# Optimization experiments

Hardware: AMD Instinct MI355X
Metric: run time of the kernel (lower is better)

## Reference

```python
import jax, jax.numpy as jnp
import numpy as np

B, N, C = 8, 1024, 768
H = 12
D = C // H  # head_dim = 64
SCALE = D ** -0.5
EPS = 1e-5


def _layer_norm(x):
    # per-head LayerNorm over last dim, gamma=1, beta=0, biased variance
    mean = x.mean(-1, keepdims=True)
    var = ((x - mean) ** 2).mean(-1, keepdims=True)
    return (x - mean) / jnp.sqrt(var + EPS)


def setup_inputs() -> dict:
    key = jax.random.key(0)
    k1, k2, k3 = jax.random.split(key, 3)
    x = jax.random.normal(k1, (B, N, C), dtype=jnp.float32)
    qkv_weight = jax.random.normal(k2, (3 * C, C), dtype=jnp.float32) * (C ** -0.5)
    proj_weight = jax.random.normal(k3, (C, C), dtype=jnp.float32) * (C ** -0.5)
    return {"x": x, "qkv_weight": qkv_weight, "proj_weight": proj_weight}


def reference(x, qkv_weight, proj_weight):
    Bx, Nx, Cx = x.shape
    qkv = x @ qkv_weight.T                          # [B,N,3C]
    qkv = qkv.reshape(Bx, Nx, 3, H, D).transpose(2, 0, 3, 1, 4)  # [3,B,H,N,D]
    q, k, v = qkv[0], qkv[1], qkv[2]
    q = _layer_norm(q) * SCALE
    k = _layer_norm(k)
    attn = jnp.einsum('bhnd,bhmd->bhnm', q, k)      # [B,H,N,N]
    attn = jax.nn.softmax(attn, axis=-1)
    out = jnp.einsum('bhnm,bhmd->bhnd', attn, v)    # [B,H,N,D]
    out = out.transpose(0, 2, 1, 3).reshape(Bx, Nx, Cx)
    return out @ proj_weight.T
```

## Files before the change

### kernel.cpp

```cpp
#include <hip/hip_runtime.h>
#include <stdint.h>
#include <stddef.h>

#define HB 8
#define HN 1024
#define HC 768
#define HH 12
#define HD 64
#define ROWS (HB*HN)
#define BH (HB*HH)

using s16x4  = __attribute__((ext_vector_type(4))) short;
using bf16x8 = __attribute__((ext_vector_type(8))) short;
using f32x4  = __attribute__((ext_vector_type(4))) float;

__device__ __forceinline__ short f2bf(float f) {
  union { float f; uint32_t u; } c; c.f = f;
  uint32_t u = c.u;
  uint32_t r = (u + 0x7fffu + ((u >> 16) & 1u)) >> 16;
  return (short)r;
}
__device__ __forceinline__ float bf2f(short s) {
  union { uint32_t u; float f; } c; c.u = ((uint32_t)(uint16_t)s) << 16;
  return c.f;
}
__device__ __forceinline__ uint32_t pack_bf16_rne(float a, float b) {
  union { float f; uint32_t u; } ca, cb; ca.f = a; cb.f = b;
  uint32_t ra = ca.u + 0x7fffu + ((ca.u >> 16) & 1u);
  uint32_t rb = cb.u + 0x7fffu + ((cb.u >> 16) & 1u);
  return __builtin_amdgcn_perm(rb, ra, 0x07060302);
}
__device__ __forceinline__ float fast_exp2(float x) {
#if __has_builtin(__builtin_amdgcn_exp2f)
  return __builtin_amdgcn_exp2f(x);
#else
  return exp2f(x);
#endif
}
__device__ __forceinline__ f32x4 mfma16(bf16x8 a, bf16x8 b, f32x4 c) {
  return __builtin_amdgcn_mfma_f32_16x16x32_bf16(a, b, c, 0, 0, 0);
}
__device__ __forceinline__ void gll16(const void* g, void* l) {
  __builtin_amdgcn_global_load_lds((const __attribute__((address_space(1))) void*)g,
                                   (__attribute__((address_space(3))) void*)l,
                                   16, 0, 0);
}

__global__ void cvt3_kernel(const float* __restrict__ x,  short* __restrict__ xb,  int n0,
                            const float* __restrict__ wq, short* __restrict__ wqb, int n1,
                            const float* __restrict__ wp, short* __restrict__ wpb, int n2) {
  int i = blockIdx.x * 256 + threadIdx.x;
  const float* in; short* out;
  if (i < n0)            { in = x;  out = xb;  }
  else if (i < n0 + n1)  { i -= n0; in = wq; out = wqb; }
  else if (i < n0 + n1 + n2) { i -= n0 + n1; in = wp; out = wpb; }
  else return;
  float4 v = ((const float4*)in)[i];
  s16x4 o;
  o.x = f2bf(v.x); o.y = f2bf(v.y); o.z = f2bf(v.z); o.w = f2bf(v.w);
  ((s16x4*)out)[i] = o;
}

template<int VM, bool STG, int SLOT>
__device__ __forceinline__ void qkv_ktile(
    int kt, short* sA, short* sB,
    const short* Ag, const short* Bg,
    int wr, int wc, int quad, int lc,
    int aoff0, int aoff1, int boff0,
    int cA0, int cA1, int cB0,
    f32x4 (&acc)[4][4])
{
  if constexpr (VM == 3) asm volatile("s_waitcnt vmcnt(3)" ::: "memory");
  else                   asm volatile("s_waitcnt vmcnt(0)" ::: "memory");
  __builtin_amdgcn_s_barrier();
  if constexpr (STG) {
    constexpr int DST = (SLOT + 2) % 3;
    const int kcol = (kt + 2) * 32;
    short* dA = sA + DST*8192;
    short* dB = sB + DST*4096;
    gll16(Ag + (size_t)(aoff0 + kcol), (void*)(dA + cA0*8));
    gll16(Ag + (size_t)(aoff1 + kcol), (void*)(dA + cA1*8));
    gll16(Bg + (size_t)(boff0 + kcol), (void*)(dB + cB0*8));
  }
  const short* sa = sA + SLOT*8192;
  const short* sb = sB + SLOT*4096;
  bf16x8 af[4], bfr[4];
#pragma unroll
  for (int mt = 0; mt < 4; ++mt) {
    const int rA = wr*64 + mt*16 + lc;
    af[mt] = *(const bf16x8*)(sa + rA*32 + (quad ^ ((rA >> 1) & 3))*8);
  }
#pragma unroll
  for (int nt = 0; nt < 4; ++nt) {
    const int rB = wc*64 + nt*16 + lc;
    bfr[nt] = *(const bf16x8*)(sb + rB*32 + (quad ^ ((rB >> 1) & 3))*8);
  }
  __builtin_amdgcn_s_setprio(1);
#pragma unroll
  for (int mt = 0; mt < 4; ++mt)
#pragma unroll
    for (int nt = 0; nt < 4; ++nt)
      acc[mt][nt] = mfma16(af[mt], bfr[nt], acc[mt][nt]);
  __builtin_amdgcn_s_setprio(0);
}

__global__ __launch_bounds__(512, 4) void gemm_qkv(const short* __restrict__ A,
                                                   const short* __restrict__ Bw,
                                                   short* __restrict__ Qb,
                                                   short* __restrict__ Kb,
                                                   short* __restrict__ Vtb) {
  __shared__ short SMEM[3*256*32 + 3*128*32];
  short* As = SMEM;
  short* Bs = SMEM + 3*256*32;
  const int wg = blockIdx.x;
  const int swz = (wg & 7)*72 + (wg >> 3);
  const int by = swz / 18, bx = swz % 18;
  const int m0 = by*256, n0 = bx*128;
  const int tid = threadIdx.x;
  const int lane = tid & 63, w = tid >> 6, quad = lane >> 4, lc = lane & 15;
  const int wr = w >> 1, wc = w & 1;
  const int cA0 = tid,        rA0 = cA0 >> 2, sbA0 = ((cA0 & 3) ^ ((rA0 >> 1) & 3))*8;
  const int cA1 = 512 + tid,  rA1 = cA1 >> 2, sbA1 = ((cA1 & 3) ^ ((rA1 >> 1) & 3))*8;
  const int cB0 = tid,        rB0 = cB0 >> 2, sbB0 = ((cB0 & 3) ^ ((rB0 >> 1) & 3))*8;
  const int aoff0 = rA0*HC + sbA0;
  const int aoff1 = rA1*HC + sbA1;
  const int boff0 = rB0*HC + sbB0;
  const short* Ag = A  + (size_t)m0*HC;
  const short* Bg = Bw + (size_t)n0*HC;
  f32x4 acc[4][4] = {};

#pragma unroll
  for (int pk = 0; pk < 2; ++pk) {
    gll16(Ag + (size_t)(aoff0 + pk*32), (void*)(As + pk*8192 + cA0*8));
    gll16(Ag + (size_t)(aoff1 + pk*32), (void*)(As + pk*8192 + cA1*8));
    gll16(Bg + (size_t)(boff0 + pk*32), (void*)(Bs + pk*4096 + cB0*8));
  }

#pragma unroll 1
  for (int kt = 0; kt < 21; kt += 3) {
    qkv_ktile<3,true,0>(kt,   As, Bs, Ag, Bg, wr, wc, quad, lc,
                        aoff0, aoff1, boff0, cA0, cA1, cB0, acc);
    qkv_ktile<3,true,1>(kt+1, As, Bs, Ag, Bg, wr, wc, quad, lc,
                        aoff0, aoff1, boff0, cA0, cA1, cB0, acc);
    qkv_ktile<3,true,2>(kt+2, As, Bs, Ag, Bg, wr, wc, quad, lc,
                        aoff0, aoff1, boff0, cA0, cA1, cB0, acc);
  }
  qkv_ktile<3,true ,0>(21, As, Bs, Ag, Bg, wr, wc, quad, lc,
                       aoff0, aoff1, boff0, cA0, cA1, cB0, acc);
  qkv_ktile<3,false,1>(22, As, Bs, Ag, Bg, wr, wc, quad, lc,
                       aoff0, aoff1, boff0, cA0, cA1, cB0, acc);
  qkv_ktile<0,false,2>(23, As, Bs, Ag, Bg, wr, wc, quad, lc,
                       aoff0, aoff1, boff0, cA0, cA1, cB0, acc);

  const int cg = n0 + wc*64;
  const int t = cg / HC;
  const int h = (cg % HC) / HD;
  if (t < 2) {
    short* outp = (t == 0) ? Qb : Kb;
    const float sc = (t == 0) ? 0.125f : 1.0f;
#pragma unroll
    for (int i = 0; i < 4; ++i)
#pragma unroll
      for (int r = 0; r < 4; ++r) {
        float s1 = (acc[i][0][r] + acc[i][1][r]) + (acc[i][2][r] + acc[i][3][r]);
        float s2 = acc[i][0][r]*acc[i][0][r];
        s2 = __builtin_fmaf(acc[i][1][r], acc[i][1][r], s2);
        s2 = __builtin_fmaf(acc[i][2][r], acc[i][2][r], s2);
        s2 = __builtin_fmaf(acc[i][3][r], acc[i][3][r], s2);
#pragma unroll
        for (int off = 1; off < 16; off <<= 1) {
          s1 += __shfl_xor(s1, off);
          s2 += __shfl_xor(s2, off);
        }
        const float mean = s1 * (1.0f/64.0f);
        const float var  = s2 * (1.0f/64.0f) - mean*mean;
        const float inv  = rsqrtf(var + 1e-5f) * sc;
        const int row = m0 + wr*64 + i*16 + quad*4 + r;
        const int b = row >> 10, n_in = row & 1023;
        short* rowp = outp + ((size_t)(b*HH + h)*HN + n_in)*HD;
#pragma unroll
        for (int nt = 0; nt < 4; ++nt)
          rowp[nt*16 + lc] = f2bf((acc[i][nt][r] - mean) * inv);
      }
  } else {
    short* vs = SMEM;
    __syncthreads();
    const int hd = wc;
#pragma unroll
    for (int i = 0; i < 4; ++i)
#pragma unroll
      for (int nt = 0; nt < 4; ++nt)
#pragma unroll
        for (int r = 0; r < 4; ++r) {
          const int dd = nt*16 + lc;
          const int k  = i*16 + quad*4 + r;
          const int c  = ((k & 15) << 2) | (k >> 4);
          vs[(hd*64 + dd)*268 + wr*64 + c] = f2bf(acc[i][nt][r]);
        }
    __syncthreads();
    const int b = m0 >> 10, m0g = m0 & 1023;
#pragma unroll
    for (int it = 0; it < 8; ++it) {
      const int idx = it*512 + tid;
      const int h2 = idx >> 11;
      const int rem = idx & 2047;
      const int dd = rem >> 5, c8 = rem & 31;
      const int habs = ((n0 + h2*64) - 1536) >> 6;
      const short* src = vs + (h2*64 + dd)*268 + c8*8;
      s16x4 lo = *(const s16x4*)(src);
      s16x4 hi = *(const s16x4*)(src + 4);
      bf16x8 vvv;
      vvv[0]=lo[0]; vvv[1]=lo[1]; vvv[2]=lo[2]; vvv[3]=lo[3];
      vvv[4]=hi[0]; vvv[5]=hi[1]; vvv[6]=hi[2]; vvv[7]=hi[3];
      *(bf16x8*)(Vtb + ((size_t)((b*HH + habs)*HD + dd))*HN + m0g + c8*8) = vvv;
    }
  }
}

template<int VM, bool STG, int SLOT>
__device__ __forceinline__ void bt_ktile(
    int kt, short* sA, short* sB,
    const short* Ag, const short* Bg,
    int wr, int wc, int quad, int lc,
    int aoff0, int aoff1, int boff0, int boff1,
    int cA0, int cA1, int cB0, int cB1,
    f32x4 (&acc)[4][4])
{
  if constexpr (VM == 4) asm volatile("s_waitcnt vmcnt(4)" ::: "memory");
  else                   asm volatile("s_waitcnt vmcnt(0)" ::: "memory");
  __builtin_amdgcn_s_barrier();
  if constexpr (STG) {
    constexpr int DST = (SLOT + 2) % 3;
    const int kcol = (kt + 2) * 32;
    short* dA = sA + DST*4096;
    short* dB = sB + DST*4096;
    gll16(Ag + (size_t)(aoff0 + kcol), (void*)(dA + cA0*8));
    gll16(Ag + (size_t)(aoff1 + kcol), (void*)(dA + cA1*8));
    gll16(Bg + (size_t)(boff0 + kcol), (void*)(dB + cB0*8));
    gll16(Bg + (size_t)(boff1 + kcol), (void*)(dB + cB1*8));
  }
  const short* sa = sA + SLOT*4096;
  const short* sb = sB + SLOT*4096;
  bf16x8 af[4], bfr[4];
#pragma unroll
  for (int mt = 0; mt < 4; ++mt) {
    const int rA = wr*64 + mt*16 + lc;
    af[mt] = *(const bf16x8*)(sa + rA*32 + (quad ^ ((rA >> 1) & 3))*8);
  }
#pragma unroll
  for (int nt = 0; nt < 4; ++nt) {
    const int rB = wc*64 + nt*16 + lc;
    bfr[nt] = *(const bf16x8*)(sb + rB*32 + (quad ^ ((rB >> 1) & 3))*8);
  }
  __builtin_amdgcn_s_setprio(1);
#pragma unroll
  for (int mt = 0; mt < 4; ++mt)
#pragma unroll
    for (int nt = 0; nt < 4; ++nt)
      acc[mt][nt] = mfma16(af[mt], bfr[nt], acc[mt][nt]);
  __builtin_amdgcn_s_setprio(0);
}

__global__ __launch_bounds__(256, 3) void gemm_bt_f32(const short* __restrict__ A,
                                                      const short* __restrict__ Bw,
                                                      float* __restrict__ C) {
  __shared__ short As[3*128*32];
  __shared__ short Bs[3*128*32];
  const int wg = blockIdx.x;
  const int swz = (wg & 7)*48 + (wg >> 3);
  const int by = swz / 6, bx = swz % 6;
  const int m0 = by*128, n0 = bx*128;
  const int tid = threadIdx.x;
  const int lane = tid & 63, w = tid >> 6, quad = lane >> 4, lc = lane & 15;
  const int wr = w >> 1, wc = w & 1;
  const int cA0 = tid,        rA0 = cA0 >> 2, sbA0 = ((cA0 & 3) ^ ((rA0 >> 1) & 3))*8;
  const int cA1 = 256 + tid,  rA1 = cA1 >> 2, sbA1 = ((cA1 & 3) ^ ((rA1 >> 1) & 3))*8;
  const int aoff0 = rA0*HC + sbA0;
  const int aoff1 = rA1*HC + sbA1;
  const int cB0 = cA0, cB1 = cA1;
  const int boff0 = aoff0, boff1 = aoff1;
  const short* Ag = A  + (size_t)m0*HC;
  const short* Bg = Bw + (size_t)n0*HC;
  f32x4 acc[4][4] = {};

#pragma unroll
  for (int pk = 0; pk < 2; ++pk) {
    gll16(Ag + (size_t)(aoff0 + pk*32), (void*)(As + pk*4096 + cA0*8));
    gll16(Ag + (size_t)(aoff1 + pk*32), (void*)(As + pk*4096 + cA1*8));
    gll16(Bg + (size_t)(boff0 + pk*32), (void*)(Bs + pk*4096 + cB0*8));
    gll16(Bg + (size_t)(boff1 + pk*32), (void*)(Bs + pk*4096 + cB1*8));
  }

#pragma unroll 1
  for (int kt = 0; kt < 21; kt += 3) {
    bt_ktile<4,true,0>(kt,   As, Bs, Ag, Bg, wr, wc, quad, lc,
                       aoff0, aoff1, boff0, boff1, cA0, cA1, cB0, cB1, acc);
    bt_ktile<4,true,1>(kt+1, As, Bs, Ag, Bg, wr, wc, quad, lc,
                       aoff0, aoff1, boff0, boff1, cA0, cA1, cB0, cB1, acc);
    bt_ktile<4,true,2>(kt+2, As, Bs, Ag, Bg, wr, wc, quad, lc,
                       aoff0, aoff1, boff0, boff1, cA0, cA1, cB0, cB1, acc);
  }
  bt_ktile<4,true ,0>(21, As, Bs, Ag, Bg, wr, wc, quad, lc,
                      aoff0, aoff1, boff0, boff1, cA0, cA1, cB0, cB1, acc);
  bt_ktile<4,false,1>(22, As, Bs, Ag, Bg, wr, wc, quad, lc,
                      aoff0, aoff1, boff0, boff1, cA0, cA1, cB0, cB1, acc);
  bt_ktile<0,false,2>(23, As, Bs, Ag, Bg, wr, wc, quad, lc,
                      aoff0, aoff1, boff0, boff1, cA0, cA1, cB0, cB1, acc);

#pragma unroll
  for (int mt = 0; mt < 4; ++mt)
#pragma unroll
    for (int nt = 0; nt < 4; ++nt)
#pragma unroll
      for (int r = 0; r < 4; ++r) {
        const int row = m0 + wr*64 + mt*16 + quad*4 + r;
        const int col = n0 + wc*64 + nt*16 + lc;
        C[(size_t)row*HC + col] = acc[mt][nt][r];
      }
}

__global__ __launch_bounds__(256, 3) void attn_kernel(const short* __restrict__ Qb,
                                                      const short* __restrict__ Kb,
                                                      const short* __restrict__ Vtb,
                                                      short* __restrict__ AOb) {
  const int raw = blockIdx.x;
  const int blk = (raw & 7)*96 + (raw >> 3);
  const int qt = blk & 7, bh = blk >> 3;
  const int b = bh / HH, h = bh % HH;
  const int tid = threadIdx.x, w = tid >> 6, lane = tid & 63;
  const int quad = lane >> 4, lc = lane & 15;

  __shared__ short Ks [64][72];
  __shared__ short Vts[64][72];
  __shared__ short Ps [4][32][72];

  bf16x8 aq[2][2];
#pragma unroll
  for (int mt = 0; mt < 2; ++mt) {
    const int mrow = qt*128 + w*32 + mt*16 + lc;
    aq[mt][0] = *(const bf16x8*)(Qb + ((size_t)bh*HN + mrow)*HD + quad*8);
    aq[mt][1] = *(const bf16x8*)(Qb + ((size_t)bh*HN + mrow)*HD + 32 + quad*8);
  }

  const short* kbh = Kb  + (size_t)bh*HN*HD;
  const short* vbh = Vtb + (size_t)bh*HD*HN;

  f32x4 oacc[2][4] = {};
  float l_i[2][4] = {};

  bf16x8 gk[2], gv[2];
#pragma unroll
  for (int i = 0; i < 2; ++i) {
    const int c = i*256 + tid;
    gk[i] = *(const bf16x8*)(kbh + (size_t)(c >> 3)*HD + (c & 7)*8);
    gv[i] = *(const bf16x8*)(vbh + (size_t)(c >> 3)*HN + (c & 7)*8);
  }
#pragma unroll
  for (int i = 0; i < 2; ++i) {
    const int c = i*256 + tid;
    *(bf16x8*)(&Ks [c >> 3][(c & 7)*8]) = gk[i];
    *(bf16x8*)(&Vts[c >> 3][(c & 7)*8]) = gv[i];
  }
  __syncthreads();

  const float LOG2E = 1.44269504f;
  const float MB2   = 8.0f * 1.44269504f;

  for (int ck = 0; ck < 16; ++ck) {
    if (ck < 15) {
      const int nn0 = (ck + 1)*64;
#pragma unroll
      for (int i = 0; i < 2; ++i) {
        const int c = i*256 + tid;
        gk[i] = *(const bf16x8*)(kbh + (size_t)(nn0 + (c >> 3))*HD + (c & 7)*8);
        gv[i] = *(const bf16x8*)(vbh + (size_t)(c >> 3)*HN + nn0 + (c & 7)*8);
      }
    }

    f32x4 sacc[2][4] = {};
#pragma unroll
    for (int kk = 0; kk < 2; ++kk)
#pragma unroll
      for (int nt = 0; nt < 4; ++nt) {
        bf16x8 bk = *(const bf16x8*)(&Ks[nt*16 + lc][kk*32 + quad*8]);
#pragma unroll
        for (int mt = 0; mt < 2; ++mt)
          sacc[mt][nt] = mfma16(aq[mt][kk], bk, sacc[mt][nt]);
      }

#pragma unroll
    for (int mt = 0; mt < 2; ++mt)
#pragma unroll
      for (int r = 0; r < 4; ++r) {
        float ps[4];
#pragma unroll
        for (int nt = 0; nt < 4; ++nt) {
          ps[nt] = fast_exp2(__builtin_fmaf(sacc[mt][nt][r], LOG2E, -MB2));
          sacc[mt][nt][r] = ps[nt];
        }
        l_i[mt][r] += (ps[0] + ps[1]) + (ps[2] + ps[3]);
        uint2 pk;
        pk.x = pack_bf16_rne(ps[0], ps[1]);
        pk.y = pack_bf16_rne(ps[2], ps[3]);
        *(uint2*)(&Ps[w][mt*16 + quad*4 + r][lc*4]) = pk;
      }

#pragma unroll
    for (int kk = 0; kk < 2; ++kk) {
      bf16x8 ap[2];
#pragma unroll
      for (int mt = 0; mt < 2; ++mt)
        ap[mt] = *(const bf16x8*)(&Ps[w][mt*16 + lc][kk*32 + quad*8]);
#pragma unroll
      for (int nt2 = 0; nt2 < 4; ++nt2) {
        bf16x8 bv = *(const bf16x8*)(&Vts[nt2*16 + lc][kk*32 + quad*8]);
#pragma unroll
        for (int mt = 0; mt < 2; ++mt)
          oacc[mt][nt2] = mfma16(ap[mt], bv, oacc[mt][nt2]);
      }
    }

    if (ck < 15) {
      __syncthreads();
#pragma unroll
      for (int i = 0; i < 2; ++i) {
        const int c = i*256 + tid;
        *(bf16x8*)(&Ks [c >> 3][(c & 7)*8]) = gk[i];
        *(bf16x8*)(&Vts[c >> 3][(c & 7)*8]) = gv[i];
      }
      __syncthreads();
    }
  }

#pragma unroll
  for (int mt = 0; mt < 2; ++mt)
#pragma unroll
    for (int r = 0; r < 4; ++r) {
      float l = l_i[mt][r];
#pragma unroll
      for (int off = 1; off < 16; off <<= 1) l += __shfl_xor(l, off);
      const float rl = 1.0f / l;
      const int row = qt*128 + w*32 + mt*16 + quad*4 + r;
#pragma unroll
      for (int nt2 = 0; nt2 < 4; ++nt2) {
        const int d = nt2*16 + lc;
        AOb[((size_t)(b*HN + row))*HC + h*HD + d] = f2bf(oacc[mt][nt2][r] * rl);
      }
    }
}

extern "C" void kernel_launch(void* const* d_in, const int* in_sizes, int n_in,
                              void* d_out, int out_size, void* d_ws, size_t ws_size,
                              hipStream_t stream) {
  const float* x     = (const float*)d_in[0];
  const float* wqkv  = (const float*)d_in[1];
  const float* wproj = (const float*)d_in[2];
  float* out = (float*)d_out;

  char* ws = (char*)d_ws;
  size_t off = 0;
  auto alloc = [&](size_t bytes) -> void* {
    void* p = ws + off; off += (bytes + 255) & ~(size_t)255; return p;
  };
  short* xb     = (short*)alloc((size_t)ROWS*HC*2);
  short* wqkvb  = (short*)alloc((size_t)3*HC*HC*2);
  short* wprojb = (short*)alloc((size_t)HC*HC*2);
  short* Qb     = (short*)alloc((size_t)BH*HN*HD*2);
  short* Kb     = (short*)alloc((size_t)BH*HN*HD*2);
  short* Vtb    = (short*)alloc((size_t)BH*HD*HN*2);
  short* AOb    = (short*)alloc((size_t)ROWS*HC*2);

  { const int n0 = ROWS*HC/4, n1 = 3*HC*HC/4, n2 = HC*HC/4;
    const int tot = n0 + n1 + n2;
    cvt3_kernel<<<(tot + 255)/256, 256, 0, stream>>>(x, xb, n0, wqkv, wqkvb, n1,
                                                     wproj, wprojb, n2); }

  gemm_qkv<<<dim3(576), 512, 0, stream>>>(xb, wqkvb, Qb, Kb, Vtb);
  attn_kernel<<<BH*8, 256, 0, stream>>>(Qb, Kb, Vtb, AOb);
  gemm_bt_f32<<<dim3(384), 256, 0, stream>>>(AOb, wprojb, out);
}
```

Before: 181.0 us.

## Fuse fp32-to-bf16 conversion of x into QKV GEMM A-tile loading

Drops the separate conversion of the activation x to bf16. The QKV GEMM now loads fp32 x tiles into registers one k-step ahead, packs them to bf16 and writes them to LDS, while B still uses direct global-to-LDS loads. This avoids writing and re-reading a bf16 copy of x. In exchange, each of the 18 column blocks that share an x row tile rereads fp32 x, which is twice the bytes of bf16. The pipeline also gains register pressure and conversion ALU work.

```diff
diff --git a/kernel.cpp b/kernel.cpp
--- a/kernel.cpp
+++ b/kernel.cpp
@@ -46,14 +46,12 @@
                                    16, 0, 0);
 }
 
-__global__ void cvt3_kernel(const float* __restrict__ x,  short* __restrict__ xb,  int n0,
-                            const float* __restrict__ wq, short* __restrict__ wqb, int n1,
-                            const float* __restrict__ wp, short* __restrict__ wpb, int n2) {
+__global__ void cvt2_kernel(const float* __restrict__ wq, short* __restrict__ wqb, int n0,
+                            const float* __restrict__ wp, short* __restrict__ wpb, int n1) {
   int i = blockIdx.x * 256 + threadIdx.x;
   const float* in; short* out;
-  if (i < n0)            { in = x;  out = xb;  }
-  else if (i < n0 + n1)  { i -= n0; in = wq; out = wqb; }
-  else if (i < n0 + n1 + n2) { i -= n0 + n1; in = wp; out = wpb; }
+  if (i < n0)            { in = wq; out = wqb; }
+  else if (i < n0 + n1)  { i -= n0; in = wp; out = wpb; }
   else return;
   float4 v = ((const float4*)in)[i];
   s16x4 o;
@@ -61,26 +59,41 @@
   ((s16x4*)out)[i] = o;
 }
 
-template<int VM, bool STG, int SLOT>
+template<int VM, bool LOADA, bool STGB, bool WRA, int SLOT>
 __device__ __forceinline__ void qkv_ktile(
     int kt, short* sA, short* sB,
-    const short* Ag, const short* Bg,
+    const float* Ax, const short* Bg,
     int wr, int wc, int quad, int lc,
-    int aoff0, int aoff1, int boff0,
+    int axoff0, int axoff1, int boff0,
     int cA0, int cA1, int cB0,
+    float4 (&av)[4],
     f32x4 (&acc)[4][4])
 {
-  if constexpr (VM == 3) asm volatile("s_waitcnt vmcnt(3)" ::: "memory");
-  else                   asm volatile("s_waitcnt vmcnt(0)" ::: "memory");
+  if constexpr (VM == 1) asm volatile("s_waitcnt vmcnt(1) lgkmcnt(0)" ::: "memory");
+  else                   asm volatile("s_waitcnt vmcnt(0) lgkmcnt(0)" ::: "memory");
   __builtin_amdgcn_s_barrier();
-  if constexpr (STG) {
-    constexpr int DST = (SLOT + 2) % 3;
-    const int kcol = (kt + 2) * 32;
+  constexpr int DST = (SLOT + 2) % 3;
+  if constexpr (WRA) {
     short* dA = sA + DST*8192;
+    uint4 w0, w1;
+    w0.x = pack_bf16_rne(av[0].x, av[0].y); w0.y = pack_bf16_rne(av[0].z, av[0].w);
+    w0.z = pack_bf16_rne(av[1].x, av[1].y); w0.w = pack_bf16_rne(av[1].z, av[1].w);
+    w1.x = pack_bf16_rne(av[2].x, av[2].y); w1.y = pack_bf16_rne(av[2].z, av[2].w);
+    w1.z = pack_bf16_rne(av[3].x, av[3].y); w1.w = pack_bf16_rne(av[3].z, av[3].w);
+    *(uint4*)(dA + cA0*8) = w0;
+    *(uint4*)(dA + cA1*8) = w1;
+  }
+  if constexpr (LOADA) {
+    const int kc = (kt + 3) * 32;
+    av[0] = *(const float4*)(Ax + axoff0 + kc);
+    av[1] = *(const float4*)(Ax + axoff0 + kc + 4);
+    av[2] = *(const float4*)(Ax + axoff1 + kc);
+    av[3] = *(const float4*)(Ax + axoff1 + kc + 4);
+  }
+  __builtin_amdgcn_sched_barrier(0);
+  if constexpr (STGB) {
     short* dB = sB + DST*4096;
-    gll16(Ag + (size_t)(aoff0 + kcol), (void*)(dA + cA0*8));
-    gll16(Ag + (size_t)(aoff1 + kcol), (void*)(dA + cA1*8));
-    gll16(Bg + (size_t)(boff0 + kcol), (void*)(dB + cB0*8));
+    gll16(Bg + (size_t)(boff0 + (kt + 2) * 32), (void*)(dB + cB0*8));
   }
   const short* sa = sA + SLOT*8192;
   const short* sb = sB + SLOT*4096;
@@ -104,7 +117,7 @@
   __builtin_amdgcn_s_setprio(0);
 }
 
-__global__ __launch_bounds__(512, 4) void gemm_qkv(const short* __restrict__ A,
+__global__ __launch_bounds__(512, 4) void gemm_qkv(const float* __restrict__ X,
                                                    const short* __restrict__ Bw,
                                                    short* __restrict__ Qb,
                                                    short* __restrict__ Kb,
@@ -122,35 +135,58 @@
   const int cA0 = tid,        rA0 = cA0 >> 2, sbA0 = ((cA0 & 3) ^ ((rA0 >> 1) & 3))*8;
   const int cA1 = 512 + tid,  rA1 = cA1 >> 2, sbA1 = ((cA1 & 3) ^ ((rA1 >> 1) & 3))*8;
   const int cB0 = tid,        rB0 = cB0 >> 2, sbB0 = ((cB0 & 3) ^ ((rB0 >> 1) & 3))*8;
-  const int aoff0 = rA0*HC + sbA0;
-  const int aoff1 = rA1*HC + sbA1;
-  const int boff0 = rB0*HC + sbB0;
-  const short* Ag = A  + (size_t)m0*HC;
+  const int axoff0 = rA0*HC + sbA0;
+  const int axoff1 = rA1*HC + sbA1;
+  const int boff0  = rB0*HC + sbB0;
+  const float* Ax = X  + (size_t)m0*HC;
   const short* Bg = Bw + (size_t)n0*HC;
   f32x4 acc[4][4] = {};
-
-#pragma unroll
-  for (int pk = 0; pk < 2; ++pk) {
-    gll16(Ag + (size_t)(aoff0 + pk*32), (void*)(As + pk*8192 + cA0*8));
-    gll16(Ag + (size_t)(aoff1 + pk*32), (void*)(As + pk*8192 + cA1*8));
-    gll16(Bg + (size_t)(boff0 + pk*32), (void*)(Bs + pk*4096 + cB0*8));
-  }
+  float4 av[4];
+
+  {
+    float4 p0[4], p1[4];
+    p0[0] = *(const float4*)(Ax + axoff0);      p0[1] = *(const float4*)(Ax + axoff0 + 4);
+    p0[2] = *(const float4*)(Ax + axoff1);      p0[3] = *(const float4*)(Ax + axoff1 + 4);
+    p1[0] = *(const float4*)(Ax + axoff0 + 32); p1[1] = *(const float4*)(Ax + axoff0 + 36);
+    p1[2] = *(const float4*)(Ax + axoff1 + 32); p1[3] = *(const float4*)(Ax + axoff1 + 36);
+    asm volatile("s_waitcnt vmcnt(0)" ::: "memory");
+#pragma unroll
+    for (int t = 0; t < 2; ++t) {
+      float4* p = t ? p1 : p0;
+      short* dA = As + t*8192;
+      uint4 w0, w1;
+      w0.x = pack_bf16_rne(p[0].x, p[0].y); w0.y = pack_bf16_rne(p[0].z, p[0].w);
+      w0.z = pack_bf16_rne(p[1].x, p[1].y); w0.w = pack_bf16_rne(p[1].z, p[1].w);
+      w1.x = pack_bf16_rne(p[2].x, p[2].y); w1.y = pack_bf16_rne(p[2].z, p[2].w);
+      w1.z = pack_bf16_rne(p[3].x, p[3].y); w1.w = pack_bf16_rne(p[3].z, p[3].w);
+      *(uint4*)(dA + cA0*8) = w0;
+      *(uint4*)(dA + cA1*8) = w1;
+    }
+  }
+  __builtin_amdgcn_sched_barrier(0);
+  av[0] = *(const float4*)(Ax + axoff0 + 64);
+  av[1] = *(const float4*)(Ax + axoff0 + 68);
+  av[2] = *(const float4*)(Ax + axoff1 + 64);
+  av[3] = *(const float4*)(Ax + axoff1 + 68);
+  __builtin_amdgcn_sched_barrier(0);
+  gll16(Bg + (size_t)(boff0 +  0), (void*)(Bs + 0*4096 + cB0*8));
+  gll16(Bg + (size_t)(boff0 + 32), (void*)(Bs + 1*4096 + cB0*8));
 
 #pragma unroll 1
   for (int kt = 0; kt < 21; kt += 3) {
-    qkv_ktile<3,true,0>(kt,   As, Bs, Ag, Bg, wr, wc, quad, lc,
-                        aoff0, aoff1, boff0, cA0, cA1, cB0, acc);
-    qkv_ktile<3,true,1>(kt+1, As, Bs, Ag, Bg, wr, wc, quad, lc,
-                        aoff0, aoff1, boff0, cA0, cA1, cB0, acc);
-    qkv_ktile<3,true,2>(kt+2, As, Bs, Ag, Bg, wr, wc, quad, lc,
-                        aoff0, aoff1, boff0, cA0, cA1, cB0, acc);
-  }
-  qkv_ktile<3,true ,0>(21, As, Bs, Ag, Bg, wr, wc, quad, lc,
-                       aoff0, aoff1, boff0, cA0, cA1, cB0, acc);
-  qkv_ktile<3,false,1>(22, As, Bs, Ag, Bg, wr, wc, quad, lc,
-                       aoff0, aoff1, boff0, cA0, cA1, cB0, acc);
-  qkv_ktile<0,false,2>(23, As, Bs, Ag, Bg, wr, wc, quad, lc,
-                       aoff0, aoff1, boff0, cA0, cA1, cB0, acc);
+    qkv_ktile<1,true,true,true,0>(kt,   As, Bs, Ax, Bg, wr, wc, quad, lc,
+                                  axoff0, axoff1, boff0, cA0, cA1, cB0, av, acc);
+    qkv_ktile<1,true,true,true,1>(kt+1, As, Bs, Ax, Bg, wr, wc, quad, lc,
+                                  axoff0, axoff1, boff0, cA0, cA1, cB0, av, acc);
+    qkv_ktile<1,true,true,true,2>(kt+2, As, Bs, Ax, Bg, wr, wc, quad, lc,
+                                  axoff0, axoff1, boff0, cA0, cA1, cB0, av, acc);
+  }
+  qkv_ktile<1,false,true ,true ,0>(21, As, Bs, Ax, Bg, wr, wc, quad, lc,
+                                   axoff0, axoff1, boff0, cA0, cA1, cB0, av, acc);
+  qkv_ktile<1,false,false,false,1>(22, As, Bs, Ax, Bg, wr, wc, quad, lc,
+                                   axoff0, axoff1, boff0, cA0, cA1, cB0, av, acc);
+  qkv_ktile<0,false,false,false,2>(23, As, Bs, Ax, Bg, wr, wc, quad, lc,
+                                   axoff0, axoff1, boff0, cA0, cA1, cB0, av, acc);
 
   const int cg = n0 + wc*64;
   const int t = cg / HC;
@@ -462,7 +498,6 @@
   auto alloc = [&](size_t bytes) -> void* {
     void* p = ws + off; off += (bytes + 255) & ~(size_t)255; return p;
   };
-  short* xb     = (short*)alloc((size_t)ROWS*HC*2);
   short* wqkvb  = (short*)alloc((size_t)3*HC*HC*2);
   short* wprojb = (short*)alloc((size_t)HC*HC*2);
   short* Qb     = (short*)alloc((size_t)BH*HN*HD*2);
@@ -470,12 +505,12 @@
   short* Vtb    = (short*)alloc((size_t)BH*HD*HN*2);
   short* AOb    = (short*)alloc((size_t)ROWS*HC*2);
 
-  { const int n0 = ROWS*HC/4, n1 = 3*HC*HC/4, n2 = HC*HC/4;
-    const int tot = n0 + n1 + n2;
-    cvt3_kernel<<<(tot + 255)/256, 256, 0, stream>>>(x, xb, n0, wqkv, wqkvb, n1,
-                                                     wproj, wprojb, n2); }
-
-  gemm_qkv<<<dim3(576), 512, 0, stream>>>(xb, wqkvb, Qb, Kb, Vtb);
+  { const int n0 = 3*HC*HC/4, n1 = HC*HC/4;
+    const int tot = n0 + n1;
+    cvt2_kernel<<<(tot + 255)/256, 256, 0, stream>>>(wqkv, wqkvb, n0,
+                                                     wproj, wprojb, n1); }
+
+  gemm_qkv<<<dim3(576), 512, 0, stream>>>(x, wqkvb, Qb, Kb, Vtb);
   attn_kernel<<<BH*8, 256, 0, stream>>>(Qb, Kb, Vtb, AOb);
   gemm_bt_f32<<<dim3(384), 256, 0, stream>>>(AOb, wprojb, out);
 }
```

Result: slower. 299.6 us (+65.5%).
